# Kernel tuning notes

Measured on AMD Instinct MI355X. Metric: run time of the kernel, lower is better.

Reference implementation:

```python
import math
import jax, jax.numpy as jnp
import numpy as np

B, S, D_MODEL, H = 2, 2048, 1024, 16
D_HEAD = D_MODEL // H
NEG = -90000000000.0


def setup_inputs() -> dict:
    key = jax.random.key(0)
    ks = jax.random.split(key, 12)
    scale = 1.0 / math.sqrt(D_MODEL)
    return {
        "Q": jax.random.normal(ks[0], (B, S, D_MODEL), jnp.float32),
        "K": jax.random.normal(ks[1], (B, S, D_MODEL), jnp.float32),
        "V": jax.random.normal(ks[2], (B, S, D_MODEL), jnp.float32),
        "mask": jax.random.randint(ks[3], (B, 1, S, S), 0, 2).astype(bool),
        "Wq": jax.random.normal(ks[4], (D_MODEL, D_MODEL), jnp.float32) * scale,
        "bq": jnp.zeros((D_MODEL,), jnp.float32),
        "Wk": jax.random.normal(ks[5], (D_MODEL, D_MODEL), jnp.float32) * scale,
        "bk": jnp.zeros((D_MODEL,), jnp.float32),
        "Wv": jax.random.normal(ks[6], (D_MODEL, D_MODEL), jnp.float32) * scale,
        "bv": jnp.zeros((D_MODEL,), jnp.float32),
        "Wo": jax.random.normal(ks[7], (D_MODEL, D_MODEL), jnp.float32) * scale,
        "bo": jnp.zeros((D_MODEL,), jnp.float32),
    }


def _split_heads(x):
    # (B, S, D) -> (B, H, S, Dh)
    b, s, _ = x.shape
    return x.reshape(b, s, H, D_HEAD).transpose(0, 2, 1, 3)


def reference(Q, K, V, mask, Wq, bq, Wk, bk, Wv, bv, Wo, bo):
    q = _split_heads(Q @ Wq.T + bq)
    k = _split_heads(K @ Wk.T + bk)
    v = _split_heads(V @ Wv.T + bv)
    # scaled dot product with additive mask (mask.float() * -9e10)
    scores = jnp.einsum("bhqd,bhkd->bhqk", q, k) / math.sqrt(D_HEAD)
    scores = scores + mask.astype(scores.dtype) * NEG
    attn = jax.nn.softmax(scores, axis=-1)
    ctx = jnp.einsum("bhqk,bhkd->bhqd", attn, v)  # (B, H, S, Dh)
    ctx = ctx.transpose(0, 2, 1, 3).reshape(Q.shape[0], q.shape[2], D_MODEL)
    return ctx @ Wo.T + bo
```

## Files before the change

kernel.cpp:

```cpp
#include <hip/hip_runtime.h>
#include <hip/hip_bf16.h>


typedef __bf16 bf16x8 __attribute__((ext_vector_type(8)));
typedef __bf16 bf16x4 __attribute__((ext_vector_type(4)));
typedef float f32x4 __attribute__((ext_vector_type(4)));

#define S_LEN 2048
#define DM 1024
#define NH 16
#define DH 64
#define MROWS 4096

#define QSCALE 0.18033688011112042f

static __device__ __forceinline__ unsigned short f2bf(float f) {
    __bf16 b = (__bf16)f;
    unsigned short u; __builtin_memcpy(&u, &b, 2); return u;
}

static __device__ __forceinline__ float exp2_hw(float x) {
#if __has_builtin(__builtin_amdgcn_exp2f)
    return __builtin_amdgcn_exp2f(x);
#else
    float r; asm("v_exp_f32 %0, %1" : "=v"(r) : "v"(x)); return r;
#endif
}

static __device__ __forceinline__ bf16x8 cvt8(float4 a, float4 b) {
    bf16x8 o;
    o[0] = (__bf16)a.x; o[1] = (__bf16)a.y; o[2] = (__bf16)a.z; o[3] = (__bf16)a.w;
    o[4] = (__bf16)b.x; o[5] = (__bf16)b.y; o[6] = (__bf16)b.z; o[7] = (__bf16)b.w;
    return o;
}

__global__ __launch_bounds__(256)
void prep(const int* __restrict__ m, unsigned* __restrict__ mb,
          const float* __restrict__ Q, unsigned short* __restrict__ dQ,
          const float* __restrict__ K, unsigned short* __restrict__ dK,
          const float* __restrict__ V, unsigned short* __restrict__ dV,
          const float* __restrict__ W0, unsigned short* __restrict__ dW0,
          const float* __restrict__ W1, unsigned short* __restrict__ dW1,
          const float* __restrict__ W2, unsigned short* __restrict__ dW2,
          const float* __restrict__ W3, unsigned short* __restrict__ dW3)
{
    const int bx = blockIdx.x, tid = threadIdx.x;
    if (bx < 1024) {
        const int lane = tid & 63, w = tid >> 6;
        const int row = bx * 4 + w;
        const int* src = m + (size_t)row * S_LEN;
        unsigned* dst = mb + (size_t)row * (S_LEN / 32);
        for (int i = 0; i < 32; i++) {
            int v = src[i * 64 + lane];
            unsigned long long bm = __ballot(v != 0);
            if (lane == 0) { dst[i*2] = (unsigned)bm; dst[i*2+1] = (unsigned)(bm >> 32); }
        }
    } else if (bx < 7168) {
        int t = bx - 1024;
        int which = t >> 11;
        const float* s = which == 0 ? Q : which == 1 ? K : V;
        unsigned short* d = which == 0 ? dQ : which == 1 ? dK : dV;
        int i = ((t & 2047) * 256 + tid) * 8;
        float4 a = *(const float4*)(s + i);
        float4 b = *(const float4*)(s + i + 4);
        *(bf16x8*)(d + i) = cvt8(a, b);
    } else {
        int t = bx - 7168;
        int which = t >> 9;
        const float* s = which == 0 ? W0 : which == 1 ? W1 : which == 2 ? W2 : W3;
        unsigned short* d = which == 0 ? dW0 : which == 1 ? dW1 : which == 2 ? dW2 : dW3;
        int i = ((t & 511) * 256 + tid) * 8;
        float4 a = *(const float4*)(s + i);
        float4 b = *(const float4*)(s + i + 4);
        *(bf16x8*)(d + i) = cvt8(a, b);
    }
}

__global__ __launch_bounds__(256)
void gemm128(const unsigned short* __restrict__ X0, const unsigned short* __restrict__ X1,
             const unsigned short* __restrict__ X2,
             const unsigned short* __restrict__ W0, const unsigned short* __restrict__ W1,
             const unsigned short* __restrict__ W2,
             const float* __restrict__ b0, const float* __restrict__ b1,
             const float* __restrict__ b2,
             unsigned short* __restrict__ d0, unsigned short* __restrict__ d1,
             unsigned short* __restrict__ d2)
{
    __shared__ __align__(16) unsigned short As[128 * 32];
    __shared__ __align__(16) unsigned short Bs[128 * 32];
    const int z = blockIdx.z;
    const unsigned short* X = z == 0 ? X0 : z == 1 ? X1 : X2;
    const unsigned short* W = z == 0 ? W0 : z == 1 ? W1 : W2;
    const float* bias        = z == 0 ? b0 : z == 1 ? b1 : b2;
    unsigned short* dstb     = z == 0 ? d0 : z == 1 ? d1 : d2;

    const int tid  = threadIdx.x;
    const int m0   = blockIdx.y * 128;
    const int n0   = blockIdx.x * 128;
    const int lane = tid & 63;
    const int w    = tid >> 6;
    const int wm   = (w >> 1) * 64, wn = (w & 1) * 64;
    const int lr   = lane & 15;
    const int lg   = lane >> 4;

    f32x4 acc[4][4];
#pragma unroll
    for (int i = 0; i < 4; i++)
#pragma unroll
        for (int j = 0; j < 4; j++) acc[i][j] = f32x4{0.f, 0.f, 0.f, 0.f};

    for (int k0 = 0; k0 < DM; k0 += 32) {
        __syncthreads();
#pragma unroll
        for (int j = 0; j < 2; j++) {
            int e = tid + j * 256;
            int row = e >> 2, c8 = (e & 3) * 8;
            __builtin_amdgcn_global_load_lds(
                (const __attribute__((address_space(1))) unsigned*)&X[(size_t)(m0 + row) * DM + k0 + c8],
                (__attribute__((address_space(3))) unsigned*)&As[e * 8], 16, 0, 0);
            __builtin_amdgcn_global_load_lds(
                (const __attribute__((address_space(1))) unsigned*)&W[(size_t)(n0 + row) * DM + k0 + c8],
                (__attribute__((address_space(3))) unsigned*)&Bs[e * 8], 16, 0, 0);
        }
        __syncthreads();
        bf16x8 af[4], bfr[4];
#pragma unroll
        for (int mi = 0; mi < 4; mi++)
            af[mi] = *(const bf16x8*)(&As[(wm + mi * 16 + lr) * 32 + lg * 8]);
#pragma unroll
        for (int ni = 0; ni < 4; ni++)
            bfr[ni] = *(const bf16x8*)(&Bs[(wn + ni * 16 + lr) * 32 + lg * 8]);
#pragma unroll
        for (int mi = 0; mi < 4; mi++)
#pragma unroll
            for (int ni = 0; ni < 4; ni++)
                acc[mi][ni] = __builtin_amdgcn_mfma_f32_16x16x32_bf16(
                    af[mi], bfr[ni], acc[mi][ni], 0, 0, 0);
    }

#pragma unroll
    for (int mi = 0; mi < 4; mi++) {
#pragma unroll
        for (int ni = 0; ni < 4; ni++) {
            const int gcol = n0 + wn + ni * 16 + lr;
            const float bv = bias[gcol];
            const int grow0 = m0 + wm + mi * 16 + lg * 4;
            if (z == 2) {
                int b = grow0 >> 11, s = grow0 & (S_LEN - 1);
                int h = gcol >> 6, dh = gcol & 63;
                bf16x4 pk;
#pragma unroll
                for (int r = 0; r < 4; r++) pk[r] = (__bf16)(acc[mi][ni][r] + bv);
                size_t di = ((size_t)(b * NH + h) * DH + dh) * S_LEN + s;
                *(bf16x4*)(&dstb[di]) = pk;
            } else {
#pragma unroll
                for (int r = 0; r < 4; r++) {
                    int grow = grow0 + r;
                    float v = acc[mi][ni][r] + bv;
                    if (z == 0) v *= QSCALE;
                    int b = grow >> 11, s = grow & (S_LEN - 1);
                    int h = gcol >> 6, dh = gcol & 63;
                    dstb[((size_t)(b * NH + h) * S_LEN + s) * DH + dh] = f2bf(v);
                }
            }
        }
    }
}

__global__ __launch_bounds__(256)
void gemm_out(const unsigned short* __restrict__ X, const unsigned short* __restrict__ W,
              const float* __restrict__ bias, float* __restrict__ dst)
{
    __shared__ __align__(16) unsigned short As[128 * 32];
    __shared__ __align__(16) unsigned short Bs[64 * 32];
    const int tid  = threadIdx.x;
    const int m0   = blockIdx.y * 128;
    const int n0   = blockIdx.x * 64;
    const int lane = tid & 63;
    const int w    = tid >> 6;
    const int wm   = (w >> 1) * 64, wn = (w & 1) * 32;
    const int lr   = lane & 15;
    const int lg   = lane >> 4;

    f32x4 acc[4][2];
#pragma unroll
    for (int i = 0; i < 4; i++)
#pragma unroll
        for (int j = 0; j < 2; j++) acc[i][j] = f32x4{0.f, 0.f, 0.f, 0.f};

    for (int k0 = 0; k0 < DM; k0 += 32) {
        __syncthreads();
#pragma unroll
        for (int j = 0; j < 2; j++) {
            int e = tid + j * 256;
            int row = e >> 2, c8 = (e & 3) * 8;
            __builtin_amdgcn_global_load_lds(
                (const __attribute__((address_space(1))) unsigned*)&X[(size_t)(m0 + row) * DM + k0 + c8],
                (__attribute__((address_space(3))) unsigned*)&As[e * 8], 16, 0, 0);
        }
        {
            int row = tid >> 2, c8 = (tid & 3) * 8;
            __builtin_amdgcn_global_load_lds(
                (const __attribute__((address_space(1))) unsigned*)&W[(size_t)(n0 + row) * DM + k0 + c8],
                (__attribute__((address_space(3))) unsigned*)&Bs[tid * 8], 16, 0, 0);
        }
        __syncthreads();
        bf16x8 af[4], bfr[2];
#pragma unroll
        for (int mi = 0; mi < 4; mi++)
            af[mi] = *(const bf16x8*)(&As[(wm + mi * 16 + lr) * 32 + lg * 8]);
#pragma unroll
        for (int ni = 0; ni < 2; ni++)
            bfr[ni] = *(const bf16x8*)(&Bs[(wn + ni * 16 + lr) * 32 + lg * 8]);
#pragma unroll
        for (int mi = 0; mi < 4; mi++)
#pragma unroll
            for (int ni = 0; ni < 2; ni++)
                acc[mi][ni] = __builtin_amdgcn_mfma_f32_16x16x32_bf16(
                    af[mi], bfr[ni], acc[mi][ni], 0, 0, 0);
    }
#pragma unroll
    for (int mi = 0; mi < 4; mi++)
#pragma unroll
        for (int ni = 0; ni < 2; ni++) {
            const int gcol = n0 + wn + ni * 16 + lr;
            const float bv = bias[gcol];
            const int grow0 = m0 + wm + mi * 16 + lg * 4;
#pragma unroll
            for (int r = 0; r < 4; r++)
                dst[(size_t)(grow0 + r) * DM + gcol] = acc[mi][ni][r] + bv;
        }
}

__global__ __launch_bounds__(256, 2)
void attn(const unsigned short* __restrict__ q_ws,
          const unsigned short* __restrict__ k_ws,
          const unsigned short* __restrict__ vt_ws,
          const unsigned* __restrict__ mbits,
          unsigned short* __restrict__ ctx)
{
    __shared__ __align__(16) unsigned short Ks[64 * 72];
    __shared__ __align__(16) unsigned short Vs[64 * 72];
    __shared__ __align__(16) unsigned short Pq[4][32 * 72];
    const int tid = threadIdx.x, lane = tid & 63, w = tid >> 6;
    const int lr = lane & 15, lg = lane >> 4;

    const int i    = blockIdx.x;
    const int xcd  = i & 7;
    const int slot = i >> 3;
    const int bh   = xcd * 4 + (slot >> 4);
    const int qblk = slot & 15;
    const int b  = bh >> 4;
    const int h  = bh & 15;
    const int q0 = qblk * 128 + w * 32;
    const int qA = q0 + lr;
    const int qB = q0 + 16 + lr;

    const int srow = tid >> 3;
    const int sseg = tid & 7;

    const unsigned short* qh = q_ws + (size_t)bh * S_LEN * DH;
    const unsigned short* kh = k_ws + (size_t)bh * S_LEN * DH;
    const unsigned short* vh = vt_ws + (size_t)bh * DH * S_LEN;
    const unsigned* mrA = mbits + (size_t)(b * S_LEN + qA) * (S_LEN / 32);
    const unsigned* mrB = mbits + (size_t)(b * S_LEN + qB) * (S_LEN / 32);

    bf16x8 aqA[2], aqB[2];
#pragma unroll
    for (int c = 0; c < 2; c++) {
        aqA[c] = *(const bf16x8*)(&qh[(size_t)qA * DH + c * 32 + lg * 8]);
        aqB[c] = *(const bf16x8*)(&qh[(size_t)qB * DH + c * 32 + lg * 8]);
    }

    bf16x8 ones;
#pragma unroll
    for (int j = 0; j < 8; j++) ones[j] = (__bf16)1.0f;

    f32x4 accA[4], accB[4], accRA, accRB;
#pragma unroll
    for (int di = 0; di < 4; di++) {
        accA[di] = f32x4{0.f, 0.f, 0.f, 0.f};
        accB[di] = f32x4{0.f, 0.f, 0.f, 0.f};
    }
    accRA = f32x4{0.f, 0.f, 0.f, 0.f};
    accRB = f32x4{0.f, 0.f, 0.f, 0.f};

    uint4 kreg0, kreg1, vreg0, vreg1;
    kreg0 = *(const uint4*)(&kh[(size_t)(srow)      * DH + sseg * 8]);
    kreg1 = *(const uint4*)(&kh[(size_t)(srow + 32) * DH + sseg * 8]);
    vreg0 = *(const uint4*)(&vh[(size_t)(srow)      * S_LEN + sseg * 8]);
    vreg1 = *(const uint4*)(&vh[(size_t)(srow + 32) * S_LEN + sseg * 8]);

    unsigned short* pq = &Pq[w][0];

    for (int it = 0; it < 32; it++) {
        const int kv0 = it * 64;
        __syncthreads();
        *(uint4*)(&Ks[(srow)      * 72 + sseg * 8]) = kreg0;
        *(uint4*)(&Ks[(srow + 32) * 72 + sseg * 8]) = kreg1;
        *(uint4*)(&Vs[(srow)      * 72 + sseg * 8]) = vreg0;
        *(uint4*)(&Vs[(srow + 32) * 72 + sseg * 8]) = vreg1;
        __syncthreads();
        if (it < 31) {
            const int kn = kv0 + 64;
            kreg0 = *(const uint4*)(&kh[(size_t)(kn + srow)      * DH + sseg * 8]);
            kreg1 = *(const uint4*)(&kh[(size_t)(kn + srow + 32) * DH + sseg * 8]);
            vreg0 = *(const uint4*)(&vh[(size_t)(srow)      * S_LEN + kn + sseg * 8]);
            vreg1 = *(const uint4*)(&vh[(size_t)(srow + 32) * S_LEN + kn + sseg * 8]);
        }

        const uint2 mwA = *(const uint2*)(&mrA[it * 2]);
        const uint2 mwB = *(const uint2*)(&mrB[it * 2]);

        f32x4 sA[4], sB[4];
#pragma unroll
        for (int ni = 0; ni < 4; ni++) {
            bf16x8 ak0 = *(const bf16x8*)(&Ks[(ni * 16 + lr) * 72 + lg * 8]);
            bf16x8 ak1 = *(const bf16x8*)(&Ks[(ni * 16 + lr) * 72 + 32 + lg * 8]);
            f32x4 tA = __builtin_amdgcn_mfma_f32_16x16x32_bf16(ak0, aqA[0], f32x4{0.f,0.f,0.f,0.f}, 0,0,0);
            tA = __builtin_amdgcn_mfma_f32_16x16x32_bf16(ak1, aqA[1], tA, 0,0,0);
            f32x4 tB = __builtin_amdgcn_mfma_f32_16x16x32_bf16(ak0, aqB[0], f32x4{0.f,0.f,0.f,0.f}, 0,0,0);
            tB = __builtin_amdgcn_mfma_f32_16x16x32_bf16(ak1, aqB[1], tB, 0,0,0);
            sA[ni] = tA; sB[ni] = tB;
        }

#pragma unroll
        for (int ni = 0; ni < 4; ni++) {
            unsigned wA = (ni & 2) ? mwA.y : mwA.x;
            unsigned wB = (ni & 2) ? mwB.y : mwB.x;
            unsigned nibA = wA >> ((ni & 1) * 16 + lg * 4);
            unsigned nibB = wB >> ((ni & 1) * 16 + lg * 4);
#pragma unroll
            for (int r = 0; r < 4; r++) {
                float pA = exp2_hw(sA[ni][r]);
                float pB = exp2_hw(sB[ni][r]);
                sA[ni][r] = (nibA & (1u << r)) ? 0.f : pA;
                sB[ni][r] = (nibB & (1u << r)) ? 0.f : pB;
            }
        }

#pragma unroll
        for (int ni = 0; ni < 4; ni++) {
            bf16x4 pkA, pkB;
#pragma unroll
            for (int r = 0; r < 4; r++) {
                pkA[r] = (__bf16)sA[ni][r];
                pkB[r] = (__bf16)sB[ni][r];
            }
            *(bf16x4*)(&pq[(lr)      * 72 + ni * 16 + lg * 4]) = pkA;
            *(bf16x4*)(&pq[(16 + lr) * 72 + ni * 16 + lg * 4]) = pkB;
        }

        bf16x8 bpA0 = *(const bf16x8*)(&pq[(lr)      * 72 + lg * 8]);
        bf16x8 bpA1 = *(const bf16x8*)(&pq[(lr)      * 72 + 32 + lg * 8]);
        bf16x8 bpB0 = *(const bf16x8*)(&pq[(16 + lr) * 72 + lg * 8]);
        bf16x8 bpB1 = *(const bf16x8*)(&pq[(16 + lr) * 72 + 32 + lg * 8]);

#pragma unroll
        for (int di = 0; di < 4; di++) {
            bf16x8 av0 = *(const bf16x8*)(&Vs[(di * 16 + lr) * 72 + lg * 8]);
            bf16x8 av1 = *(const bf16x8*)(&Vs[(di * 16 + lr) * 72 + 32 + lg * 8]);
            accA[di] = __builtin_amdgcn_mfma_f32_16x16x32_bf16(av0, bpA0, accA[di], 0, 0, 0);
            accA[di] = __builtin_amdgcn_mfma_f32_16x16x32_bf16(av1, bpA1, accA[di], 0, 0, 0);
            accB[di] = __builtin_amdgcn_mfma_f32_16x16x32_bf16(av0, bpB0, accB[di], 0, 0, 0);
            accB[di] = __builtin_amdgcn_mfma_f32_16x16x32_bf16(av1, bpB1, accB[di], 0, 0, 0);
        }

        accRA = __builtin_amdgcn_mfma_f32_16x16x32_bf16(ones, bpA0, accRA, 0, 0, 0);
        accRA = __builtin_amdgcn_mfma_f32_16x16x32_bf16(ones, bpA1, accRA, 0, 0, 0);
        accRB = __builtin_amdgcn_mfma_f32_16x16x32_bf16(ones, bpB0, accRB, 0, 0, 0);
        accRB = __builtin_amdgcn_mfma_f32_16x16x32_bf16(ones, bpB1, accRB, 0, 0, 0);
    }

    const float invA = 1.0f / fmaxf(accRA[0], 1e-37f);
    const float invB = 1.0f / fmaxf(accRB[0], 1e-37f);

    unsigned short* crowA = &ctx[((size_t)(b * S_LEN + qA)) * DM + h * DH];
    unsigned short* crowB = &ctx[((size_t)(b * S_LEN + qB)) * DM + h * DH];
#pragma unroll
    for (int di = 0; di < 4; di++) {
        bf16x4 oA, oB;
#pragma unroll
        for (int r = 0; r < 4; r++) {
            oA[r] = (__bf16)(accA[di][r] * invA);
            oB[r] = (__bf16)(accB[di][r] * invB);
        }
        *(bf16x4*)(&crowA[di * 16 + lg * 4]) = oA;
        *(bf16x4*)(&crowB[di * 16 + lg * 4]) = oB;
    }
}

extern "C" void kernel_launch(void* const* d_in, const int* in_sizes, int n_in,
                              void* d_out, int out_size, void* d_ws, size_t ws_size,
                              hipStream_t stream)
{
    (void)in_sizes; (void)n_in; (void)out_size; (void)ws_size;
    const float* Q  = (const float*)d_in[0];
    const float* K  = (const float*)d_in[1];
    const float* V  = (const float*)d_in[2];
    const int*   Mk = (const int*)d_in[3];
    const float* Wq = (const float*)d_in[4];
    const float* bq = (const float*)d_in[5];
    const float* Wk = (const float*)d_in[6];
    const float* bk = (const float*)d_in[7];
    const float* Wv = (const float*)d_in[8];
    const float* bv = (const float*)d_in[9];
    const float* Wo = (const float*)d_in[10];
    const float* bo = (const float*)d_in[11];

    const int NX = MROWS * DM;
    const int NW = DM * DM;

    unsigned short* q_ws  = (unsigned short*)d_ws;
    unsigned short* k_ws  = q_ws + (size_t)NX;
    unsigned short* vt_ws = k_ws + (size_t)NX;
    unsigned short* ctx   = vt_ws + (size_t)NX;
    unsigned*       mbits = (unsigned*)(ctx + (size_t)NX);
    unsigned short* Wbq   = (unsigned short*)(mbits + (size_t)MROWS * (S_LEN / 32));
    unsigned short* Wbk   = Wbq + (size_t)NW;
    unsigned short* Wbv   = Wbk + (size_t)NW;
    unsigned short* Wbo   = Wbv + (size_t)NW;
    unsigned short* Xbq   = Wbo + (size_t)NW;
    unsigned short* Xbk   = Xbq + (size_t)NX;
    unsigned short* Xbv   = Xbk + (size_t)NX;
    float* out = (float*)d_out;

    dim3 blk(256);
    prep<<<dim3(9216), blk, 0, stream>>>(Mk, mbits, Q, Xbq, K, Xbk, V, Xbv,
                                         Wq, Wbq, Wk, Wbk, Wv, Wbv, Wo, Wbo);

    gemm128<<<dim3(8, 32, 3), blk, 0, stream>>>(Xbq, Xbk, Xbv, Wbq, Wbk, Wbv,
                                                bq, bk, bv, q_ws, k_ws, vt_ws);

    attn<<<dim3(512), blk, 0, stream>>>(q_ws, k_ws, vt_ws, mbits, ctx);

    gemm_out<<<dim3(16, 32), blk, 0, stream>>>(ctx, Wbo, bo, out);
}
```

Before: 272.7 us.

## Double-buffer K/V tiles in attention and vectorize GEMM epilogue stores

The attention kernel now keeps two LDS buffers for K and V and prefetches two tiles ahead. This cuts the two barriers per iteration down to one, so the next tile's LDS store overlaps with the current tile's compute. The QKV and output GEMMs swap the MFMA operands so each lane holds four consecutive columns, which allows vectorized bf16x4/float4 stores and float4 bias loads instead of scalar strided writes. The cost is twice the K/V LDS footprint, which may pressure occupancy at 2 blocks per CU, plus an extra register set kept live across the loop.

Result: slower. 298.8 us (+9.6%).

```diff
diff --git a/kernel.cpp b/kernel.cpp
--- a/kernel.cpp
+++ b/kernel.cpp
@@ -130,22 +130,31 @@
 #pragma unroll
         for (int ni = 0; ni < 4; ni++)
             bfr[ni] = *(const bf16x8*)(&Bs[(wn + ni * 16 + lr) * 32 + lg * 8]);
-#pragma unroll
-        for (int mi = 0; mi < 4; mi++)
-#pragma unroll
-            for (int ni = 0; ni < 4; ni++)
-                acc[mi][ni] = __builtin_amdgcn_mfma_f32_16x16x32_bf16(
-                    af[mi], bfr[ni], acc[mi][ni], 0, 0, 0);
-    }
-
-#pragma unroll
-    for (int mi = 0; mi < 4; mi++) {
-#pragma unroll
-        for (int ni = 0; ni < 4; ni++) {
-            const int gcol = n0 + wn + ni * 16 + lr;
-            const float bv = bias[gcol];
-            const int grow0 = m0 + wm + mi * 16 + lg * 4;
-            if (z == 2) {
+        if (z == 2) {
+#pragma unroll
+            for (int mi = 0; mi < 4; mi++)
+#pragma unroll
+                for (int ni = 0; ni < 4; ni++)
+                    acc[mi][ni] = __builtin_amdgcn_mfma_f32_16x16x32_bf16(
+                        af[mi], bfr[ni], acc[mi][ni], 0, 0, 0);
+        } else {
+#pragma unroll
+            for (int mi = 0; mi < 4; mi++)
+#pragma unroll
+                for (int ni = 0; ni < 4; ni++)
+                    acc[mi][ni] = __builtin_amdgcn_mfma_f32_16x16x32_bf16(
+                        bfr[ni], af[mi], acc[mi][ni], 0, 0, 0);
+        }
+    }
+
+    if (z == 2) {
+#pragma unroll
+        for (int mi = 0; mi < 4; mi++) {
+#pragma unroll
+            for (int ni = 0; ni < 4; ni++) {
+                const int gcol = n0 + wn + ni * 16 + lr;
+                const float bv = bias[gcol];
+                const int grow0 = m0 + wm + mi * 16 + lg * 4;
                 int b = grow0 >> 11, s = grow0 & (S_LEN - 1);
                 int h = gcol >> 6, dh = gcol & 63;
                 bf16x4 pk;
@@ -153,16 +162,26 @@
                 for (int r = 0; r < 4; r++) pk[r] = (__bf16)(acc[mi][ni][r] + bv);
                 size_t di = ((size_t)(b * NH + h) * DH + dh) * S_LEN + s;
                 *(bf16x4*)(&dstb[di]) = pk;
-            } else {
+            }
+        }
+    } else {
+#pragma unroll
+        for (int mi = 0; mi < 4; mi++) {
+            const int gm = m0 + wm + mi * 16 + lr;
+            const int b = gm >> 11, s = gm & (S_LEN - 1);
+#pragma unroll
+            for (int ni = 0; ni < 4; ni++) {
+                const int nb = n0 + wn + ni * 16 + lg * 4;
+                const float4 b4 = *(const float4*)(&bias[nb]);
+                const int h = nb >> 6, dh = nb & 63;
+                bf16x4 pk;
 #pragma unroll
                 for (int r = 0; r < 4; r++) {
-                    int grow = grow0 + r;
-                    float v = acc[mi][ni][r] + bv;
+                    float v = acc[mi][ni][r] + ((const float*)&b4)[r];
                     if (z == 0) v *= QSCALE;
-                    int b = grow >> 11, s = grow & (S_LEN - 1);
-                    int h = gcol >> 6, dh = gcol & 63;
-                    dstb[((size_t)(b * NH + h) * S_LEN + s) * DH + dh] = f2bf(v);
+                    pk[r] = (__bf16)v;
                 }
+                *(bf16x4*)(&dstb[((size_t)(b * NH + h) * S_LEN + s) * DH + dh]) = pk;
             }
         }
     }
@@ -218,19 +237,23 @@
 #pragma unroll
             for (int ni = 0; ni < 2; ni++)
                 acc[mi][ni] = __builtin_amdgcn_mfma_f32_16x16x32_bf16(
-                    af[mi], bfr[ni], acc[mi][ni], 0, 0, 0);
-    }
-#pragma unroll
-    for (int mi = 0; mi < 4; mi++)
+                    bfr[ni], af[mi], acc[mi][ni], 0, 0, 0);
+    }
+#pragma unroll
+    for (int mi = 0; mi < 4; mi++) {
+        const int gm = m0 + wm + mi * 16 + lr;
 #pragma unroll
         for (int ni = 0; ni < 2; ni++) {
-            const int gcol = n0 + wn + ni * 16 + lr;
-            const float bv = bias[gcol];
-            const int grow0 = m0 + wm + mi * 16 + lg * 4;
-#pragma unroll
-            for (int r = 0; r < 4; r++)
-                dst[(size_t)(grow0 + r) * DM + gcol] = acc[mi][ni][r] + bv;
-        }
+            const int nb = n0 + wn + ni * 16 + lg * 4;
+            const float4 b4 = *(const float4*)(&bias[nb]);
+            float4 o;
+            o.x = acc[mi][ni][0] + b4.x;
+            o.y = acc[mi][ni][1] + b4.y;
+            o.z = acc[mi][ni][2] + b4.z;
+            o.w = acc[mi][ni][3] + b4.w;
+            *(float4*)(&dst[(size_t)gm * DM + nb]) = o;
+        }
+    }
 }
 
 __global__ __launch_bounds__(256, 2)
@@ -240,8 +263,8 @@
           const unsigned* __restrict__ mbits,
           unsigned short* __restrict__ ctx)
 {
-    __shared__ __align__(16) unsigned short Ks[64 * 72];
-    __shared__ __align__(16) unsigned short Vs[64 * 72];
+    __shared__ __align__(16) unsigned short Ks[2][64 * 72];
+    __shared__ __align__(16) unsigned short Vs[2][64 * 72];
     __shared__ __align__(16) unsigned short Pq[4][32 * 72];
     const int tid = threadIdx.x, lane = tid & 63, w = tid >> 6;
     const int lr = lane & 15, lg = lane >> 4;
@@ -291,19 +314,32 @@
     kreg1 = *(const uint4*)(&kh[(size_t)(srow + 32) * DH + sseg * 8]);
     vreg0 = *(const uint4*)(&vh[(size_t)(srow)      * S_LEN + sseg * 8]);
     vreg1 = *(const uint4*)(&vh[(size_t)(srow + 32) * S_LEN + sseg * 8]);
+    *(uint4*)(&Ks[0][(srow)      * 72 + sseg * 8]) = kreg0;
+    *(uint4*)(&Ks[0][(srow + 32) * 72 + sseg * 8]) = kreg1;
+    *(uint4*)(&Vs[0][(srow)      * 72 + sseg * 8]) = vreg0;
+    *(uint4*)(&Vs[0][(srow + 32) * 72 + sseg * 8]) = vreg1;
+    kreg0 = *(const uint4*)(&kh[(size_t)(64 + srow)      * DH + sseg * 8]);
+    kreg1 = *(const uint4*)(&kh[(size_t)(64 + srow + 32) * DH + sseg * 8]);
+    vreg0 = *(const uint4*)(&vh[(size_t)(srow)      * S_LEN + 64 + sseg * 8]);
+    vreg1 = *(const uint4*)(&vh[(size_t)(srow + 32) * S_LEN + 64 + sseg * 8]);
+    __syncthreads();
 
     unsigned short* pq = &Pq[w][0];
 
     for (int it = 0; it < 32; it++) {
-        const int kv0 = it * 64;
-        __syncthreads();
-        *(uint4*)(&Ks[(srow)      * 72 + sseg * 8]) = kreg0;
-        *(uint4*)(&Ks[(srow + 32) * 72 + sseg * 8]) = kreg1;
-        *(uint4*)(&Vs[(srow)      * 72 + sseg * 8]) = vreg0;
-        *(uint4*)(&Vs[(srow + 32) * 72 + sseg * 8]) = vreg1;
-        __syncthreads();
+        const int cur = it & 1;
+        const unsigned short* Kc = &Ks[cur][0];
+        const unsigned short* Vc = &Vs[cur][0];
         if (it < 31) {
-            const int kn = kv0 + 64;
+            unsigned short* Kn = &Ks[cur ^ 1][0];
+            unsigned short* Vn = &Vs[cur ^ 1][0];
+            *(uint4*)(&Kn[(srow)      * 72 + sseg * 8]) = kreg0;
+            *(uint4*)(&Kn[(srow + 32) * 72 + sseg * 8]) = kreg1;
+            *(uint4*)(&Vn[(srow)      * 72 + sseg * 8]) = vreg0;
+            *(uint4*)(&Vn[(srow + 32) * 72 + sseg * 8]) = vreg1;
+        }
+        if (it < 30) {
+            const int kn = (it + 2) * 64;
             kreg0 = *(const uint4*)(&kh[(size_t)(kn + srow)      * DH + sseg * 8]);
             kreg1 = *(const uint4*)(&kh[(size_t)(kn + srow + 32) * DH + sseg * 8]);
             vreg0 = *(const uint4*)(&vh[(size_t)(srow)      * S_LEN + kn + sseg * 8]);
@@ -316,8 +352,8 @@
         f32x4 sA[4], sB[4];
 #pragma unroll
         for (int ni = 0; ni < 4; ni++) {
-            bf16x8 ak0 = *(const bf16x8*)(&Ks[(ni * 16 + lr) * 72 + lg * 8]);
-            bf16x8 ak1 = *(const bf16x8*)(&Ks[(ni * 16 + lr) * 72 + 32 + lg * 8]);
+            bf16x8 ak0 = *(const bf16x8*)(&Kc[(ni * 16 + lr) * 72 + lg * 8]);
+            bf16x8 ak1 = *(const bf16x8*)(&Kc[(ni * 16 + lr) * 72 + 32 + lg * 8]);
             f32x4 tA = __builtin_amdgcn_mfma_f32_16x16x32_bf16(ak0, aqA[0], f32x4{0.f,0.f,0.f,0.f}, 0,0,0);
             tA = __builtin_amdgcn_mfma_f32_16x16x32_bf16(ak1, aqA[1], tA, 0,0,0);
             f32x4 tB = __builtin_amdgcn_mfma_f32_16x16x32_bf16(ak0, aqB[0], f32x4{0.f,0.f,0.f,0.f}, 0,0,0);
@@ -359,8 +395,8 @@
 
 #pragma unroll
         for (int di = 0; di < 4; di++) {
-            bf16x8 av0 = *(const bf16x8*)(&Vs[(di * 16 + lr) * 72 + lg * 8]);
-            bf16x8 av1 = *(const bf16x8*)(&Vs[(di * 16 + lr) * 72 + 32 + lg * 8]);
+            bf16x8 av0 = *(const bf16x8*)(&Vc[(di * 16 + lr) * 72 + lg * 8]);
+            bf16x8 av1 = *(const bf16x8*)(&Vc[(di * 16 + lr) * 72 + 32 + lg * 8]);
             accA[di] = __builtin_amdgcn_mfma_f32_16x16x32_bf16(av0, bpA0, accA[di], 0, 0, 0);
             accA[di] = __builtin_amdgcn_mfma_f32_16x16x32_bf16(av1, bpA1, accA[di], 0, 0, 0);
             accB[di] = __builtin_amdgcn_mfma_f32_16x16x32_bf16(av0, bpB0, accB[di], 0, 0, 0);
@@ -371,6 +407,8 @@
         accRA = __builtin_amdgcn_mfma_f32_16x16x32_bf16(ones, bpA1, accRA, 0, 0, 0);
         accRB = __builtin_amdgcn_mfma_f32_16x16x32_bf16(ones, bpB0, accRB, 0, 0, 0);
         accRB = __builtin_amdgcn_mfma_f32_16x16x32_bf16(ones, bpB1, accRB, 0, 0, 0);
+
+        __syncthreads();
     }
 
     const float invA = 1.0f / fmaxf(accRA[0], 1e-37f);
```

## Double-buffer attention K/V tiles, shrink P scratch, and remap GEMM blocks per XCD

Applied to the files above, without the earlier changes.

The attention kernel now double-buffers K and V in shared memory. It prefetches two tiles ahead and needs one barrier per iteration instead of two. The per-wave P scratch is halved by processing the A and B query halves one after the other, and the occupancy hint rises to 3 blocks per CU. Both GEMM kernels remap the linear block id so that consecutive blocks on the same XCD share M tiles, for better L2 reuse, and gemm_out gets a 4-block occupancy hint. The risks are register pressure from the extra V fragments under the tighter launch bounds, and extra LDS traffic from reusing the same scratch serially.

After: 265.0 us. -2.8%, faster.

```diff
diff --git a/kernel.cpp b/kernel.cpp
--- a/kernel.cpp
+++ b/kernel.cpp
@@ -88,15 +88,23 @@
 {
     __shared__ __align__(16) unsigned short As[128 * 32];
     __shared__ __align__(16) unsigned short Bs[128 * 32];
-    const int z = blockIdx.z;
+
+    const int bid = blockIdx.x + blockIdx.y * 8 + blockIdx.z * 256;
+    const int xcd = bid & 7;
+    const int t   = bid >> 3;
+    const int z   = t >> 5;
+    const int u   = t & 31;
+    const int nt  = u & 7;
+    const int mt  = xcd * 4 + (u >> 3);
+
     const unsigned short* X = z == 0 ? X0 : z == 1 ? X1 : X2;
     const unsigned short* W = z == 0 ? W0 : z == 1 ? W1 : W2;
     const float* bias        = z == 0 ? b0 : z == 1 ? b1 : b2;
     unsigned short* dstb     = z == 0 ? d0 : z == 1 ? d1 : d2;
 
     const int tid  = threadIdx.x;
-    const int m0   = blockIdx.y * 128;
-    const int n0   = blockIdx.x * 128;
+    const int m0   = mt * 128;
+    const int n0   = nt * 128;
     const int lane = tid & 63;
     const int w    = tid >> 6;
     const int wm   = (w >> 1) * 64, wn = (w & 1) * 64;
@@ -168,15 +176,22 @@
     }
 }
 
-__global__ __launch_bounds__(256)
+__global__ __launch_bounds__(256, 4)
 void gemm_out(const unsigned short* __restrict__ X, const unsigned short* __restrict__ W,
               const float* __restrict__ bias, float* __restrict__ dst)
 {
     __shared__ __align__(16) unsigned short As[128 * 32];
     __shared__ __align__(16) unsigned short Bs[64 * 32];
+
+    const int bid = blockIdx.x + blockIdx.y * 16;
+    const int xcd = bid & 7;
+    const int u   = bid >> 3;
+    const int nt  = u & 15;
+    const int mt  = xcd * 4 + (u >> 4);
+
     const int tid  = threadIdx.x;
-    const int m0   = blockIdx.y * 128;
-    const int n0   = blockIdx.x * 64;
+    const int m0   = mt * 128;
+    const int n0   = nt * 64;
     const int lane = tid & 63;
     const int w    = tid >> 6;
     const int wm   = (w >> 1) * 64, wn = (w & 1) * 32;
@@ -233,16 +248,16 @@
         }
 }
 
-__global__ __launch_bounds__(256, 2)
+__global__ __launch_bounds__(256, 3)
 void attn(const unsigned short* __restrict__ q_ws,
           const unsigned short* __restrict__ k_ws,
           const unsigned short* __restrict__ vt_ws,
           const unsigned* __restrict__ mbits,
           unsigned short* __restrict__ ctx)
 {
-    __shared__ __align__(16) unsigned short Ks[64 * 72];
-    __shared__ __align__(16) unsigned short Vs[64 * 72];
-    __shared__ __align__(16) unsigned short Pq[4][32 * 72];
+    __shared__ __align__(16) unsigned short Ks[2][64 * 72];
+    __shared__ __align__(16) unsigned short Vs[2][64 * 72];
+    __shared__ __align__(16) unsigned short Pq[4][16 * 72];
     const int tid = threadIdx.x, lane = tid & 63, w = tid >> 6;
     const int lr = lane & 15, lg = lane >> 4;
 
@@ -291,19 +306,32 @@
     kreg1 = *(const uint4*)(&kh[(size_t)(srow + 32) * DH + sseg * 8]);
     vreg0 = *(const uint4*)(&vh[(size_t)(srow)      * S_LEN + sseg * 8]);
     vreg1 = *(const uint4*)(&vh[(size_t)(srow + 32) * S_LEN + sseg * 8]);
+    *(uint4*)(&Ks[0][(srow)      * 72 + sseg * 8]) = kreg0;
+    *(uint4*)(&Ks[0][(srow + 32) * 72 + sseg * 8]) = kreg1;
+    *(uint4*)(&Vs[0][(srow)      * 72 + sseg * 8]) = vreg0;
+    *(uint4*)(&Vs[0][(srow + 32) * 72 + sseg * 8]) = vreg1;
+    kreg0 = *(const uint4*)(&kh[(size_t)(64 + srow)      * DH + sseg * 8]);
+    kreg1 = *(const uint4*)(&kh[(size_t)(64 + srow + 32) * DH + sseg * 8]);
+    vreg0 = *(const uint4*)(&vh[(size_t)(srow)      * S_LEN + 64 + sseg * 8]);
+    vreg1 = *(const uint4*)(&vh[(size_t)(srow + 32) * S_LEN + 64 + sseg * 8]);
+    __syncthreads();
 
     unsigned short* pq = &Pq[w][0];
 
     for (int it = 0; it < 32; it++) {
-        const int kv0 = it * 64;
-        __syncthreads();
-        *(uint4*)(&Ks[(srow)      * 72 + sseg * 8]) = kreg0;
-        *(uint4*)(&Ks[(srow + 32) * 72 + sseg * 8]) = kreg1;
-        *(uint4*)(&Vs[(srow)      * 72 + sseg * 8]) = vreg0;
-        *(uint4*)(&Vs[(srow + 32) * 72 + sseg * 8]) = vreg1;
-        __syncthreads();
+        const int cur = it & 1;
+        const unsigned short* Kc = &Ks[cur][0];
+        const unsigned short* Vc = &Vs[cur][0];
         if (it < 31) {
-            const int kn = kv0 + 64;
+            unsigned short* Kn = &Ks[cur ^ 1][0];
+            unsigned short* Vn = &Vs[cur ^ 1][0];
+            *(uint4*)(&Kn[(srow)      * 72 + sseg * 8]) = kreg0;
+            *(uint4*)(&Kn[(srow + 32) * 72 + sseg * 8]) = kreg1;
+            *(uint4*)(&Vn[(srow)      * 72 + sseg * 8]) = vreg0;
+            *(uint4*)(&Vn[(srow + 32) * 72 + sseg * 8]) = vreg1;
+        }
+        if (it < 30) {
+            const int kn = (it + 2) * 64;
             kreg0 = *(const uint4*)(&kh[(size_t)(kn + srow)      * DH + sseg * 8]);
             kreg1 = *(const uint4*)(&kh[(size_t)(kn + srow + 32) * DH + sseg * 8]);
             vreg0 = *(const uint4*)(&vh[(size_t)(srow)      * S_LEN + kn + sseg * 8]);
@@ -316,8 +344,8 @@
         f32x4 sA[4], sB[4];
 #pragma unroll
         for (int ni = 0; ni < 4; ni++) {
-            bf16x8 ak0 = *(const bf16x8*)(&Ks[(ni * 16 + lr) * 72 + lg * 8]);
-            bf16x8 ak1 = *(const bf16x8*)(&Ks[(ni * 16 + lr) * 72 + 32 + lg * 8]);
+            bf16x8 ak0 = *(const bf16x8*)(&Kc[(ni * 16 + lr) * 72 + lg * 8]);
+            bf16x8 ak1 = *(const bf16x8*)(&Kc[(ni * 16 + lr) * 72 + 32 + lg * 8]);
             f32x4 tA = __builtin_amdgcn_mfma_f32_16x16x32_bf16(ak0, aqA[0], f32x4{0.f,0.f,0.f,0.f}, 0,0,0);
             tA = __builtin_amdgcn_mfma_f32_16x16x32_bf16(ak1, aqA[1], tA, 0,0,0);
             f32x4 tB = __builtin_amdgcn_mfma_f32_16x16x32_bf16(ak0, aqB[0], f32x4{0.f,0.f,0.f,0.f}, 0,0,0);
@@ -340,37 +368,44 @@
             }
         }
 
+        bf16x8 av0[4], av1[4];
 #pragma unroll
         for (int ni = 0; ni < 4; ni++) {
-            bf16x4 pkA, pkB;
-#pragma unroll
-            for (int r = 0; r < 4; r++) {
-                pkA[r] = (__bf16)sA[ni][r];
-                pkB[r] = (__bf16)sB[ni][r];
-            }
-            *(bf16x4*)(&pq[(lr)      * 72 + ni * 16 + lg * 4]) = pkA;
-            *(bf16x4*)(&pq[(16 + lr) * 72 + ni * 16 + lg * 4]) = pkB;
-        }
-
-        bf16x8 bpA0 = *(const bf16x8*)(&pq[(lr)      * 72 + lg * 8]);
-        bf16x8 bpA1 = *(const bf16x8*)(&pq[(lr)      * 72 + 32 + lg * 8]);
-        bf16x8 bpB0 = *(const bf16x8*)(&pq[(16 + lr) * 72 + lg * 8]);
-        bf16x8 bpB1 = *(const bf16x8*)(&pq[(16 + lr) * 72 + 32 + lg * 8]);
-
+            bf16x4 pkA;
+#pragma unroll
+            for (int r = 0; r < 4; r++) pkA[r] = (__bf16)sA[ni][r];
+            *(bf16x4*)(&pq[lr * 72 + ni * 16 + lg * 4]) = pkA;
+        }
+        bf16x8 bpA0 = *(const bf16x8*)(&pq[lr * 72 + lg * 8]);
+        bf16x8 bpA1 = *(const bf16x8*)(&pq[lr * 72 + 32 + lg * 8]);
 #pragma unroll
         for (int di = 0; di < 4; di++) {
-            bf16x8 av0 = *(const bf16x8*)(&Vs[(di * 16 + lr) * 72 + lg * 8]);
-            bf16x8 av1 = *(const bf16x8*)(&Vs[(di * 16 + lr) * 72 + 32 + lg * 8]);
-            accA[di] = __builtin_amdgcn_mfma_f32_16x16x32_bf16(av0, bpA0, accA[di], 0, 0, 0);
-            accA[di] = __builtin_amdgcn_mfma_f32_16x16x32_bf16(av1, bpA1, accA[di], 0, 0, 0);
-            accB[di] = __builtin_amdgcn_mfma_f32_16x16x32_bf16(av0, bpB0, accB[di], 0, 0, 0);
-            accB[di] = __builtin_amdgcn_mfma_f32_16x16x32_bf16(av1, bpB1, accB[di], 0, 0, 0);
-        }
-
+            av0[di] = *(const bf16x8*)(&Vc[(di * 16 + lr) * 72 + lg * 8]);
+            av1[di] = *(const bf16x8*)(&Vc[(di * 16 + lr) * 72 + 32 + lg * 8]);
+            accA[di] = __builtin_amdgcn_mfma_f32_16x16x32_bf16(av0[di], bpA0, accA[di], 0, 0, 0);
+            accA[di] = __builtin_amdgcn_mfma_f32_16x16x32_bf16(av1[di], bpA1, accA[di], 0, 0, 0);
+        }
         accRA = __builtin_amdgcn_mfma_f32_16x16x32_bf16(ones, bpA0, accRA, 0, 0, 0);
         accRA = __builtin_amdgcn_mfma_f32_16x16x32_bf16(ones, bpA1, accRA, 0, 0, 0);
+
+#pragma unroll
+        for (int ni = 0; ni < 4; ni++) {
+            bf16x4 pkB;
+#pragma unroll
+            for (int r = 0; r < 4; r++) pkB[r] = (__bf16)sB[ni][r];
+            *(bf16x4*)(&pq[lr * 72 + ni * 16 + lg * 4]) = pkB;
+        }
+        bf16x8 bpB0 = *(const bf16x8*)(&pq[lr * 72 + lg * 8]);
+        bf16x8 bpB1 = *(const bf16x8*)(&pq[lr * 72 + 32 + lg * 8]);
+#pragma unroll
+        for (int di = 0; di < 4; di++) {
+            accB[di] = __builtin_amdgcn_mfma_f32_16x16x32_bf16(av0[di], bpB0, accB[di], 0, 0, 0);
+            accB[di] = __builtin_amdgcn_mfma_f32_16x16x32_bf16(av1[di], bpB1, accB[di], 0, 0, 0);
+        }
         accRB = __builtin_amdgcn_mfma_f32_16x16x32_bf16(ones, bpB0, accRB, 0, 0, 0);
         accRB = __builtin_amdgcn_mfma_f32_16x16x32_bf16(ones, bpB1, accRB, 0, 0, 0);
+
+        __syncthreads();
     }
 
     const float invA = 1.0f / fmaxf(accRA[0], 1e-37f);
```
